# Kernel optimization log

Measured on AMD Instinct MI355X. Metric: run time of the kernel, lower is better.

The kernel has to match this reference:

```python
import jax, jax.numpy as jnp
import numpy as np

N = 50000
E = 800000
IN_DIM = 512
HID = 256
LAT = 128
K = 10
ALPHA = 0.1
BN_EPS = 1e-5


def setup_inputs() -> dict:
    key = jax.random.key(0)
    ks = jax.random.split(key, 6)
    x = jax.random.normal(ks[0], (N, IN_DIM), dtype=jnp.float32)
    edge_index = jax.random.randint(ks[1], (2, E), 0, N, dtype=jnp.int64)
    W_proj = jax.random.normal(ks[2], (IN_DIM, LAT), dtype=jnp.float32) * (IN_DIM ** -0.5)
    W1 = jax.random.normal(ks[3], (LAT, HID), dtype=jnp.float32) * (LAT ** -0.5)
    W2 = jax.random.normal(ks[4], (HID, LAT), dtype=jnp.float32) * (HID ** -0.5)
    return {
        "x": x, "edge_index": edge_index, "W_proj": W_proj,
        "W1": W1, "b1": jnp.zeros((HID,), jnp.float32),
        "gamma1": jnp.ones((HID,), jnp.float32), "beta1": jnp.zeros((HID,), jnp.float32),
        "mean1": jnp.zeros((HID,), jnp.float32), "var1": jnp.ones((HID,), jnp.float32),
        "W2": W2, "b2": jnp.zeros((LAT,), jnp.float32),
        "gamma2": jnp.ones((LAT,), jnp.float32), "beta2": jnp.zeros((LAT,), jnp.float32),
        "mean2": jnp.zeros((LAT,), jnp.float32), "var2": jnp.ones((LAT,), jnp.float32),
    }


def _gcn_norm(edge_index, n):
    # add self-loops, symmetric normalization D^-1/2 A D^-1/2 (PyG gcn_norm)
    loops = jnp.arange(n, dtype=edge_index.dtype)
    src = jnp.concatenate([edge_index[0], loops])
    dst = jnp.concatenate([edge_index[1], loops])
    deg = jax.ops.segment_sum(jnp.ones_like(dst, jnp.float32), dst, num_segments=n)
    dinv = jax.lax.rsqrt(jnp.maximum(deg, 1.0))  # deg >= 1 with self-loops
    norm = dinv[src] * dinv[dst]
    return src, dst, norm


def _propagate(h, src, dst, norm, n):
    # gather -> scale -> scatter-add: out[dst] += norm * h[src]
    return jax.ops.segment_sum(h[src] * norm[:, None], dst, num_segments=n)


def _bn(h, gamma, beta, mean, var):
    # BatchNorm1d in eval mode (running stats)
    return (h - mean) * jax.lax.rsqrt(var + BN_EPS) * gamma + beta


def reference(x, edge_index, W_proj, W1, b1, gamma1, beta1, mean1, var1,
              W2, b2, gamma2, beta2, mean2, var2):
    n = x.shape[0]
    src, dst, norm = _gcn_norm(edge_index, n)

    z0 = x @ W_proj                                   # [N, LAT]
    h1 = _propagate(z0 @ W1, src, dst, norm, n) + b1  # GCNConv 1
    h1 = jax.nn.relu(_bn(h1, gamma1, beta1, mean1, var1))
    h2 = _propagate(h1 @ W2, src, dst, norm, n) + b2  # GCNConv 2
    h2 = jax.nn.relu(_bn(h2, gamma2, beta2, mean2, var2))

    # APPNP: h_k = (1-alpha) * A_hat h_{k-1} + alpha * h_0
    def step(h, _):
        h = (1.0 - ALPHA) * _propagate(h, src, dst, norm, n) + ALPHA * h2
        return h, None
    z_refined, _ = jax.lax.scan(step, h2, None, length=K)

    z = z_refined + z0
    row, col = edge_index[0], edge_index[1]
    adj = jax.nn.sigmoid(jnp.sum(z[row] * z[col], axis=1))  # [E]
    return adj, z
```

## Files before the change

kernel.cpp:

```cpp
#include <hip/hip_runtime.h>

#define N_NODES 50000
#define N_EDGES 800000
#define IN_DIM  512
#define HID     256
#define LAT     128
#define K_ITERS 10
#define BN_EPS  1e-5f

typedef __attribute__((ext_vector_type(8))) short bf16x8;
typedef __attribute__((ext_vector_type(4))) float f32x4;

__device__ inline float bflo(unsigned v) { return __builtin_bit_cast(float, v << 16); }
__device__ inline float bfhi(unsigned v) { return __builtin_bit_cast(float, v & 0xffff0000u); }
__device__ inline unsigned f2bf_bits(float f)
{
    unsigned u = __builtin_bit_cast(unsigned, f);
    return (u + 0x7fffu + ((u >> 16) & 1u)) >> 16;
}
__device__ inline unsigned packbf(float x, float y)
{
    return f2bf_bits(x) | (f2bf_bits(y) << 16);
}

__global__ void detect_dtype_kernel(const int* __restrict__ ei32, int* __restrict__ flag)
{
    __shared__ int any;
    if (threadIdx.x == 0) any = 0;
    __syncthreads();
    int local = 0;
    for (int i = threadIdx.x; i < 4096; i += blockDim.x)
        local |= ei32[2 * i + 1];
    if (local) atomicOr(&any, 1);
    __syncthreads();
    if (threadIdx.x == 0) flag[0] = (any != 0) ? 1 : 0;
}

__global__ void init_cnt_kernel(int* __restrict__ cnt, int n)
{
    int i = blockIdx.x * blockDim.x + threadIdx.x;
    if (i < n) cnt[i] = 1;
}

__global__ void convert_count_kernel(const void* __restrict__ ei, const int* __restrict__ flag,
                                     int* __restrict__ srcE, int* __restrict__ dstE,
                                     int* __restrict__ cnt, int E)
{
    int e = blockIdx.x * blockDim.x + threadIdx.x;
    if (e >= E) return;
    int s, d;
    if (*flag) {
        const int* p = (const int*)ei;
        s = p[e]; d = p[E + e];
    } else {
        const long long* p = (const long long*)ei;
        s = (int)p[e]; d = (int)p[E + e];
    }
    srcE[e] = s;
    dstE[e] = d;
    atomicAdd(&cnt[d], 1);
}

__global__ __launch_bounds__(256) void block_sum_kernel(const int* __restrict__ cnt,
                                                        int* __restrict__ bsum, int n)
{
    __shared__ int s[256];
    int i = blockIdx.x * 256 + threadIdx.x;
    s[threadIdx.x] = (i < n) ? cnt[i] : 0;
    __syncthreads();
    for (int off = 128; off > 0; off >>= 1) {
        if (threadIdx.x < off) s[threadIdx.x] += s[threadIdx.x + off];
        __syncthreads();
    }
    if (threadIdx.x == 0) bsum[blockIdx.x] = s[0];
}

__global__ __launch_bounds__(256) void block_scan_kernel(int* __restrict__ bsum, int nb)
{
    __shared__ int s[256];
    int t = threadIdx.x;
    int v = (t < nb) ? bsum[t] : 0;
    s[t] = v;
    __syncthreads();
    for (int off = 1; off < 256; off <<= 1) {
        int u = (t >= off) ? s[t - off] : 0;
        __syncthreads();
        s[t] += u;
        __syncthreads();
    }
    if (t < nb) bsum[t] = s[t] - v;
}

__global__ __launch_bounds__(256) void final_scan_kernel(const int* __restrict__ cnt,
                                                         const int* __restrict__ bsum,
                                                         int* __restrict__ rowoff,
                                                         int* __restrict__ cursor,
                                                         float* __restrict__ dinv, int n)
{
    __shared__ int s[256];
    int t = threadIdx.x;
    int i = blockIdx.x * 256 + t;
    int c = (i < n) ? cnt[i] : 0;
    s[t] = c;
    __syncthreads();
    for (int off = 1; off < 256; off <<= 1) {
        int u = (t >= off) ? s[t - off] : 0;
        __syncthreads();
        s[t] += u;
        __syncthreads();
    }
    if (i < n) {
        int excl = bsum[blockIdx.x] + s[t] - c;
        rowoff[i] = excl;
        cursor[i] = excl;
        dinv[i] = rsqrtf((float)c);
    }
    if (i == 0) rowoff[n] = N_EDGES + N_NODES;
}

__global__ void scatter_kernel(const int* __restrict__ srcE, const int* __restrict__ dstE,
                               const float* __restrict__ dinv, int* __restrict__ cursor,
                               uint2* __restrict__ csr, int E, int n)
{
    int e = blockIdx.x * blockDim.x + threadIdx.x;
    if (e >= E + n) return;
    int s, d;
    if (e < E) { s = srcE[e]; d = dstE[e]; }
    else       { s = e - E;   d = s; }
    int pos = atomicAdd(&cursor[d], 1);
    float w = dinv[s] * dinv[d];
    csr[pos] = make_uint2((unsigned)s, __builtin_bit_cast(unsigned, w));
}

__global__ void transpose_cvt_kernel(const float* __restrict__ in, unsigned short* __restrict__ out,
                                     int R, int C)
{
    int idx = blockIdx.x * 256 + threadIdx.x;
    if (idx >= R * C) return;
    int c = idx / R, r = idx - c * R;
    out[idx] = (unsigned short)f2bf_bits(in[r * C + c]);
}

template<int KDIM, int COLS, int EPI, bool AF32>
__global__ __launch_bounds__(256) void gemm_mfma(const void* __restrict__ Ain,
                                                 const unsigned short* __restrict__ Bt,
                                                 unsigned short* __restrict__ Cout,
                                                 int M, int Nc,
                                                 const float* __restrict__ cb,
                                                 const float* __restrict__ cg,
                                                 const float* __restrict__ cbe,
                                                 const float* __restrict__ cm,
                                                 const float* __restrict__ cv)
{
    const int wave = threadIdx.x >> 6;
    const int lane = threadIdx.x & 63;
    const int s  = lane & 15;
    const int kc = lane >> 4;
    const int wrow0   = blockIdx.y * 64 + wave * 16;
    const int colbase = blockIdx.x * (16 * COLS);

    f32x4 acc[COLS] = {};

    const int arow = wrow0 + s;
    const bool aok = arow < M;

#pragma unroll 2
    for (int k0 = 0; k0 < KDIM; k0 += 32) {
        bf16x8 af = {};
        if (AF32) {
            if (aok) {
                const float* Ar = (const float*)Ain + (size_t)arow * KDIM + k0 + 8 * kc;
                float4 u0 = *(const float4*)Ar;
                float4 u1 = *(const float4*)(Ar + 4);
                af[0] = (short)f2bf_bits(u0.x); af[1] = (short)f2bf_bits(u0.y);
                af[2] = (short)f2bf_bits(u0.z); af[3] = (short)f2bf_bits(u0.w);
                af[4] = (short)f2bf_bits(u1.x); af[5] = (short)f2bf_bits(u1.y);
                af[6] = (short)f2bf_bits(u1.z); af[7] = (short)f2bf_bits(u1.w);
            }
        } else {
            if (aok)
                af = *(const bf16x8*)&((const unsigned short*)Ain)[(size_t)arow * KDIM + k0 + 8 * kc];
        }
#pragma unroll
        for (int t = 0; t < COLS; ++t) {
            const int bn = colbase + t * 16 + s;
            bf16x8 bf = *(const bf16x8*)&Bt[(size_t)bn * KDIM + k0 + 8 * kc];
            acc[t] = __builtin_amdgcn_mfma_f32_16x16x32_bf16(af, bf, acc[t], 0, 0, 0);
        }
    }

#pragma unroll
    for (int t = 0; t < COLS; ++t) {
        const int col = colbase + t * 16 + s;
        float sc = 1.f, sh = 0.f;
        if (EPI == 1) {
            sc = cg[col] * rsqrtf(cv[col] + BN_EPS);
            sh = (cb[col] - cm[col]) * sc + cbe[col];
        }
#pragma unroll
        for (int j = 0; j < 4; ++j) {
            const int crow = wrow0 + kc * 4 + j;
            if (crow < M) {
                float xv = acc[t][j];
                if (EPI == 1) xv = fmaxf(fmaf(xv, sc, sh), 0.f);
                Cout[(size_t)crow * Nc + col] = (unsigned short)f2bf_bits(xv);
            }
        }
    }
}

template<int MODE>
__global__ __launch_bounds__(256) void prop_row(const unsigned* __restrict__ in,
                                                const int* __restrict__ rowoff,
                                                const unsigned long long* __restrict__ csr,
                                                const unsigned* __restrict__ h2h,
                                                const unsigned* __restrict__ z0h,
                                                float* __restrict__ outf,
                                                unsigned* __restrict__ outh,
                                                const float* __restrict__ bb,
                                                const float* __restrict__ bg,
                                                const float* __restrict__ bbe,
                                                const float* __restrict__ bm,
                                                const float* __restrict__ bv)
{
    const int node = blockIdx.x * 4 + (threadIdx.x >> 6);
    const int lane = threadIdx.x & 63;
    const int g = lane >> 4, s = lane & 15;
    const int e0 = rowoff[node], e1 = rowoff[node + 1];

    float f[8] = {};
    int e = e0 + g;
    while (e < e1) {
        unsigned long long P[6];
        uint4 V[6];
#pragma unroll
        for (int i = 0; i < 6; ++i) { P[i] = 0; V[i] = make_uint4(0u, 0u, 0u, 0u); }
#pragma unroll
        for (int i = 0; i < 6; ++i)
            if (e + 4 * i < e1) P[i] = __builtin_nontemporal_load(&csr[e + 4 * i]);
#pragma unroll
        for (int i = 0; i < 6; ++i)
            if (e + 4 * i < e1) V[i] = *(const uint4*)&in[(size_t)(unsigned)P[i] * 64 + 4 * s];
#pragma unroll
        for (int i = 0; i < 6; ++i) {
            const float w = __builtin_bit_cast(float, (unsigned)(P[i] >> 32));
            f[0] = fmaf(w, bflo(V[i].x), f[0]); f[1] = fmaf(w, bfhi(V[i].x), f[1]);
            f[2] = fmaf(w, bflo(V[i].y), f[2]); f[3] = fmaf(w, bfhi(V[i].y), f[3]);
            f[4] = fmaf(w, bflo(V[i].z), f[4]); f[5] = fmaf(w, bfhi(V[i].z), f[5]);
            f[6] = fmaf(w, bflo(V[i].w), f[6]); f[7] = fmaf(w, bfhi(V[i].w), f[7]);
        }
        e += 24;
    }
#pragma unroll
    for (int i = 0; i < 8; ++i) {
        f[i] += __shfl_xor(f[i], 16, 64);
        f[i] += __shfl_xor(f[i], 32, 64);
    }

    if (g == 0) {
        const size_t o = (size_t)node * 64 + 4 * s;
        uint4 ov;
        if (MODE == 0) {
            ov.x = packbf(f[0], f[1]); ov.y = packbf(f[2], f[3]);
            ov.z = packbf(f[4], f[5]); ov.w = packbf(f[6], f[7]);
            *(uint4*)&outh[o] = ov;
        } else if (MODE == 1) {
            float4 G0 = *(const float4*)&bg[8 * s],  G1 = *(const float4*)&bg[8 * s + 4];
            float4 V0 = *(const float4*)&bv[8 * s],  V1 = *(const float4*)&bv[8 * s + 4];
            float4 B0 = *(const float4*)&bb[8 * s],  B1 = *(const float4*)&bb[8 * s + 4];
            float4 M0 = *(const float4*)&bm[8 * s],  M1 = *(const float4*)&bm[8 * s + 4];
            float4 E0 = *(const float4*)&bbe[8 * s], E1 = *(const float4*)&bbe[8 * s + 4];
            float gg[8] = {G0.x, G0.y, G0.z, G0.w, G1.x, G1.y, G1.z, G1.w};
            float vv[8] = {V0.x, V0.y, V0.z, V0.w, V1.x, V1.y, V1.z, V1.w};
            float bbv[8] = {B0.x, B0.y, B0.z, B0.w, B1.x, B1.y, B1.z, B1.w};
            float mm[8] = {M0.x, M0.y, M0.z, M0.w, M1.x, M1.y, M1.z, M1.w};
            float ee[8] = {E0.x, E0.y, E0.z, E0.w, E1.x, E1.y, E1.z, E1.w};
            float r[8];
#pragma unroll
            for (int i = 0; i < 8; ++i) {
                float sc = gg[i] * rsqrtf(vv[i] + BN_EPS);
                float sh = (bbv[i] - mm[i]) * sc + ee[i];
                r[i] = fmaxf(fmaf(f[i], sc, sh), 0.f);
            }
            ov.x = packbf(r[0], r[1]); ov.y = packbf(r[2], r[3]);
            ov.z = packbf(r[4], r[5]); ov.w = packbf(r[6], r[7]);
            *(uint4*)&outh[o] = ov;
        } else if (MODE == 2) {
            uint4 hv = *(const uint4*)&h2h[o];
            ov.x = packbf(fmaf(0.9f, f[0], 0.1f * bflo(hv.x)), fmaf(0.9f, f[1], 0.1f * bfhi(hv.x)));
            ov.y = packbf(fmaf(0.9f, f[2], 0.1f * bflo(hv.y)), fmaf(0.9f, f[3], 0.1f * bfhi(hv.y)));
            ov.z = packbf(fmaf(0.9f, f[4], 0.1f * bflo(hv.z)), fmaf(0.9f, f[5], 0.1f * bfhi(hv.z)));
            ov.w = packbf(fmaf(0.9f, f[6], 0.1f * bflo(hv.w)), fmaf(0.9f, f[7], 0.1f * bfhi(hv.w)));
            *(uint4*)&outh[o] = ov;
        } else {
            uint4 hv = *(const uint4*)&h2h[o];
            uint4 zv = *(const uint4*)&z0h[o];
            float r[8];
            r[0] = fmaf(0.9f, f[0], 0.1f * bflo(hv.x)) + bflo(zv.x);
            r[1] = fmaf(0.9f, f[1], 0.1f * bfhi(hv.x)) + bfhi(zv.x);
            r[2] = fmaf(0.9f, f[2], 0.1f * bflo(hv.y)) + bflo(zv.y);
            r[3] = fmaf(0.9f, f[3], 0.1f * bfhi(hv.y)) + bfhi(zv.y);
            r[4] = fmaf(0.9f, f[4], 0.1f * bflo(hv.z)) + bflo(zv.z);
            r[5] = fmaf(0.9f, f[5], 0.1f * bfhi(hv.z)) + bfhi(zv.z);
            r[6] = fmaf(0.9f, f[6], 0.1f * bflo(hv.w)) + bflo(zv.w);
            r[7] = fmaf(0.9f, f[7], 0.1f * bfhi(hv.w)) + bfhi(zv.w);
            *(float4*)&outf[(size_t)node * LAT + 8 * s]     = make_float4(r[0], r[1], r[2], r[3]);
            *(float4*)&outf[(size_t)node * LAT + 8 * s + 4] = make_float4(r[4], r[5], r[6], r[7]);
            ov.x = packbf(r[0], r[1]); ov.y = packbf(r[2], r[3]);
            ov.z = packbf(r[4], r[5]); ov.w = packbf(r[6], r[7]);
            *(uint4*)&outh[o] = ov;
        }
    }
}

__global__ __launch_bounds__(256) void edge_dot_mfma(const unsigned* __restrict__ zh,
                                                     const int* __restrict__ srcE,
                                                     const int* __restrict__ dstE,
                                                     float* __restrict__ adj)
{
    const int gw = blockIdx.x * 4 + (threadIdx.x >> 6);
    const int base = gw * 16;
    const int lane = threadIdx.x & 63;
    const int s = lane & 15, kc = lane >> 4;
    const int r = srcE[base + s];
    const int c = dstE[base + s];
    const unsigned* zr = &zh[(size_t)r * 64 + 4 * kc];
    const unsigned* zc = &zh[(size_t)c * 64 + 4 * kc];
    f32x4 acc = {};
#pragma unroll
    for (int k0 = 0; k0 < 4; ++k0) {
        bf16x8 af = *(const bf16x8*)(zr + 16 * k0);
        bf16x8 bf = *(const bf16x8*)(zc + 16 * k0);
        acc = __builtin_amdgcn_mfma_f32_16x16x32_bf16(af, bf, acc, 0, 0, 0);
    }
    if ((s >> 2) == kc) {
        const int j = s & 3;
        float v = (j == 0) ? acc[0] : (j == 1) ? acc[1] : (j == 2) ? acc[2] : acc[3];
        adj[base + s] = 1.f / (1.f + expf(-v));
    }
}

extern "C" void kernel_launch(void* const* d_in, const int* in_sizes, int n_in,
                              void* d_out, int out_size, void* d_ws, size_t ws_size,
                              hipStream_t stream)
{
    const float* x     = (const float*)d_in[0];
    const void*  ei    = d_in[1];
    const float* Wproj = (const float*)d_in[2];
    const float* W1    = (const float*)d_in[3];
    const float* b1    = (const float*)d_in[4];
    const float* g1    = (const float*)d_in[5];
    const float* be1   = (const float*)d_in[6];
    const float* m1    = (const float*)d_in[7];
    const float* v1    = (const float*)d_in[8];
    const float* W2    = (const float*)d_in[9];
    const float* b2    = (const float*)d_in[10];
    const float* g2    = (const float*)d_in[11];
    const float* be2   = (const float*)d_in[12];
    const float* m2    = (const float*)d_in[13];
    const float* v2    = (const float*)d_in[14];

    float* out_adj = (float*)d_out;
    float* out_z   = (float*)d_out + N_EDGES;

    char* w = (char*)d_ws;
    size_t off = 0;
    auto alloc = [&](size_t bytes) {
        void* p = w + off;
        off += (bytes + 255) & ~(size_t)255;
        return p;
    };
    const size_t NB = (size_t)N_NODES * 64 * 4;
    const int NBLK = (N_NODES + 255) / 256;

    int*            flag   = (int*)           alloc(4);
    int*            cnt    = (int*)           alloc((size_t)N_NODES * 4);
    int*            cursor = (int*)           alloc((size_t)N_NODES * 4);
    int*            rowoff = (int*)           alloc((size_t)(N_NODES + 1) * 4);
    float*          dinv   = (float*)         alloc((size_t)N_NODES * 4);
    int*            bsum   = (int*)           alloc(256 * 4);
    int*            srcE   = (int*)           alloc((size_t)N_EDGES * 4);
    int*            dstE   = (int*)           alloc((size_t)N_EDGES * 4);
    uint2*          csr    = (uint2*)         alloc((size_t)(N_EDGES + N_NODES) * 8);
    unsigned short* Wpt    = (unsigned short*)alloc((size_t)LAT * IN_DIM * 2);
    unsigned short* W1t    = (unsigned short*)alloc((size_t)HID * LAT * 2);
    unsigned short* W2t    = (unsigned short*)alloc((size_t)LAT * HID * 2);
    unsigned*       z0h    = (unsigned*)      alloc(NB);
    unsigned*       p0h    = (unsigned*)      alloc(NB);
    unsigned short* h1h    = (unsigned short*)alloc(2 * NB);
    unsigned*       t2h    = (unsigned*)      alloc(NB);
    unsigned*       h2h    = (unsigned*)      alloc(NB);

    unsigned* pingA = (unsigned*)h1h;
    unsigned* pingB = (unsigned*)h1h + N_NODES * 64;

    detect_dtype_kernel<<<1, 256, 0, stream>>>((const int*)ei, flag);
    init_cnt_kernel<<<(N_NODES + 255) / 256, 256, 0, stream>>>(cnt, N_NODES);
    convert_count_kernel<<<(N_EDGES + 255) / 256, 256, 0, stream>>>(ei, flag, srcE, dstE, cnt, N_EDGES);
    block_sum_kernel<<<NBLK, 256, 0, stream>>>(cnt, bsum, N_NODES);
    block_scan_kernel<<<1, 256, 0, stream>>>(bsum, NBLK);
    final_scan_kernel<<<NBLK, 256, 0, stream>>>(cnt, bsum, rowoff, cursor, dinv, N_NODES);
    scatter_kernel<<<(N_EDGES + N_NODES + 255) / 256, 256, 0, stream>>>(srcE, dstE, dinv, cursor,
                                                                        csr, N_EDGES, N_NODES);

    transpose_cvt_kernel<<<(IN_DIM * LAT + 255) / 256, 256, 0, stream>>>(Wproj, Wpt, IN_DIM, LAT);
    transpose_cvt_kernel<<<(LAT * HID + 255) / 256, 256, 0, stream>>>(W1, W1t, LAT, HID);
    transpose_cvt_kernel<<<(HID * LAT + 255) / 256, 256, 0, stream>>>(W2, W2t, HID, LAT);

    const int gy = (N_NODES + 63) / 64;
    const int pgrid = N_NODES / 4;

    gemm_mfma<IN_DIM, 4, 0, true><<<dim3(2, gy), 256, 0, stream>>>(x, Wpt, (unsigned short*)z0h,
                                                                   N_NODES, LAT,
                                                                   nullptr, nullptr, nullptr, nullptr, nullptr);
    prop_row<0><<<pgrid, 256, 0, stream>>>(z0h, rowoff, (const unsigned long long*)csr,
                                           nullptr, nullptr, nullptr, p0h,
                                           nullptr, nullptr, nullptr, nullptr, nullptr);
    gemm_mfma<LAT, 4, 1, false><<<dim3(4, gy), 256, 0, stream>>>(p0h, W1t, h1h, N_NODES, HID,
                                                                 b1, g1, be1, m1, v1);
    gemm_mfma<HID, 4, 0, false><<<dim3(2, gy), 256, 0, stream>>>(h1h, W2t, (unsigned short*)t2h,
                                                                 N_NODES, LAT,
                                                                 nullptr, nullptr, nullptr, nullptr, nullptr);
    prop_row<1><<<pgrid, 256, 0, stream>>>(t2h, rowoff, (const unsigned long long*)csr,
                                           nullptr, nullptr, nullptr, h2h,
                                           b2, g2, be2, m2, v2);

    const unsigned* cur = h2h;
    for (int it = 0; it < K_ITERS; ++it) {
        if (it == K_ITERS - 1) {
            prop_row<3><<<pgrid, 256, 0, stream>>>(cur, rowoff, (const unsigned long long*)csr,
                                                   h2h, z0h, out_z, z0h,
                                                   nullptr, nullptr, nullptr, nullptr, nullptr);
        } else {
            unsigned* nxt = (it & 1) ? pingB : pingA;
            prop_row<2><<<pgrid, 256, 0, stream>>>(cur, rowoff, (const unsigned long long*)csr,
                                                   h2h, nullptr, nullptr, nxt,
                                                   nullptr, nullptr, nullptr, nullptr, nullptr);
            cur = nxt;
        }
    }

    edge_dot_mfma<<<N_EDGES / 64, 256, 0, stream>>>(z0h, srcE, dstE, out_adj);
}
```

Before: 769.0 us.

## Software-pipeline GEMM loads with register prefetch and widen column tile

Replaces the GEMM kernel with a version in which each wave computes 8 column tiles (128 columns) rather than 4. It prefetches several A k-slices into registers and double-buffers the B fragments so global loads overlap the MFMA work. Out-of-range A rows are clamped instead of branched on, and the grids shrink to match. Separately, the CSR load in the propagation kernel switches from a nontemporal load to a normal cached load. The changes trade higher register pressure, and possibly lower occupancy, for better latency hiding and half as many redundant A reads.

```diff
diff --git a/kernel.cpp b/kernel.cpp
--- a/kernel.cpp
+++ b/kernel.cpp
@@ -141,8 +141,8 @@
     out[idx] = (unsigned short)f2bf_bits(in[r * C + c]);
 }
 
-template<int KDIM, int COLS, int EPI, bool AF32>
-__global__ __launch_bounds__(256) void gemm_mfma(const void* __restrict__ Ain,
+template<int KDIM, int EPI, bool AF32>
+__global__ __launch_bounds__(256) void gemm_pipe(const void* __restrict__ Ain,
                                                  const unsigned short* __restrict__ Bt,
                                                  unsigned short* __restrict__ Cout,
                                                  int M, int Nc,
@@ -152,45 +152,69 @@
                                                  const float* __restrict__ cm,
                                                  const float* __restrict__ cv)
 {
+    constexpr int NK = KDIM / 32;
+    constexpr int PREF = AF32 ? (NK < 4 ? NK : 4) : (NK < 8 ? NK : 8);
     const int wave = threadIdx.x >> 6;
     const int lane = threadIdx.x & 63;
     const int s  = lane & 15;
     const int kc = lane >> 4;
     const int wrow0   = blockIdx.y * 64 + wave * 16;
-    const int colbase = blockIdx.x * (16 * COLS);
-
-    f32x4 acc[COLS] = {};
-
-    const int arow = wrow0 + s;
-    const bool aok = arow < M;
-
-#pragma unroll 2
-    for (int k0 = 0; k0 < KDIM; k0 += 32) {
-        bf16x8 af = {};
-        if (AF32) {
-            if (aok) {
-                const float* Ar = (const float*)Ain + (size_t)arow * KDIM + k0 + 8 * kc;
-                float4 u0 = *(const float4*)Ar;
-                float4 u1 = *(const float4*)(Ar + 4);
-                af[0] = (short)f2bf_bits(u0.x); af[1] = (short)f2bf_bits(u0.y);
-                af[2] = (short)f2bf_bits(u0.z); af[3] = (short)f2bf_bits(u0.w);
-                af[4] = (short)f2bf_bits(u1.x); af[5] = (short)f2bf_bits(u1.y);
-                af[6] = (short)f2bf_bits(u1.z); af[7] = (short)f2bf_bits(u1.w);
+    const int colbase = blockIdx.x * 128;
+    int arow = wrow0 + s; if (arow > M - 1) arow = M - 1;
+
+    const float*          Af = (const float*)Ain + (size_t)arow * KDIM + 8 * kc;
+    const unsigned short* Ah = (const unsigned short*)Ain + (size_t)arow * KDIM + 8 * kc;
+    const unsigned short* Bp = Bt + (size_t)(colbase + s) * KDIM + 8 * kc;
+
+    float4 Araw[AF32 ? PREF : 1][2];
+    bf16x8 Areg[AF32 ? 1 : PREF];
+    bf16x8 Breg[2][8];
+    f32x4  acc[8] = {};
+
+#pragma unroll
+    for (int i = 0; i < PREF; ++i) {
+        if constexpr (AF32) {
+            Araw[i][0] = *(const float4*)(Af + 32 * i);
+            Araw[i][1] = *(const float4*)(Af + 32 * i + 4);
+        } else {
+            Areg[i] = *(const bf16x8*)(Ah + 32 * i);
+        }
+    }
+#pragma unroll
+    for (int t = 0; t < 8; ++t)
+        Breg[0][t] = *(const bf16x8*)(Bp + (size_t)16 * t * KDIM);
+
+#pragma unroll
+    for (int k = 0; k < NK; ++k) {
+        if (k + 1 < NK) {
+#pragma unroll
+            for (int t = 0; t < 8; ++t)
+                Breg[(k + 1) & 1][t] = *(const bf16x8*)(Bp + (size_t)16 * t * KDIM + 32 * (k + 1));
+        }
+        bf16x8 af;
+        if constexpr (AF32) {
+            float4 u0 = Araw[k % PREF][0];
+            float4 u1 = Araw[k % PREF][1];
+            if (k + PREF < NK) {
+                Araw[k % PREF][0] = *(const float4*)(Af + 32 * (k + PREF));
+                Araw[k % PREF][1] = *(const float4*)(Af + 32 * (k + PREF) + 4);
             }
+            af[0] = (short)f2bf_bits(u0.x); af[1] = (short)f2bf_bits(u0.y);
+            af[2] = (short)f2bf_bits(u0.z); af[3] = (short)f2bf_bits(u0.w);
+            af[4] = (short)f2bf_bits(u1.x); af[5] = (short)f2bf_bits(u1.y);
+            af[6] = (short)f2bf_bits(u1.z); af[7] = (short)f2bf_bits(u1.w);
         } else {
-            if (aok)
-                af = *(const bf16x8*)&((const unsigned short*)Ain)[(size_t)arow * KDIM + k0 + 8 * kc];
-        }
-#pragma unroll
-        for (int t = 0; t < COLS; ++t) {
-            const int bn = colbase + t * 16 + s;
-            bf16x8 bf = *(const bf16x8*)&Bt[(size_t)bn * KDIM + k0 + 8 * kc];
-            acc[t] = __builtin_amdgcn_mfma_f32_16x16x32_bf16(af, bf, acc[t], 0, 0, 0);
-        }
-    }
-
-#pragma unroll
-    for (int t = 0; t < COLS; ++t) {
+            af = Areg[k % PREF];
+            if (k + PREF < NK)
+                Areg[k % PREF] = *(const bf16x8*)(Ah + 32 * (k + PREF));
+        }
+#pragma unroll
+        for (int t = 0; t < 8; ++t)
+            acc[t] = __builtin_amdgcn_mfma_f32_16x16x32_bf16(af, Breg[k & 1][t], acc[t], 0, 0, 0);
+    }
+
+#pragma unroll
+    for (int t = 0; t < 8; ++t) {
         const int col = colbase + t * 16 + s;
         float sc = 1.f, sh = 0.f;
         if (EPI == 1) {
@@ -237,7 +261,7 @@
         for (int i = 0; i < 6; ++i) { P[i] = 0; V[i] = make_uint4(0u, 0u, 0u, 0u); }
 #pragma unroll
         for (int i = 0; i < 6; ++i)
-            if (e + 4 * i < e1) P[i] = __builtin_nontemporal_load(&csr[e + 4 * i]);
+            if (e + 4 * i < e1) P[i] = csr[e + 4 * i];
 #pragma unroll
         for (int i = 0; i < 6; ++i)
             if (e + 4 * i < e1) V[i] = *(const uint4*)&in[(size_t)(unsigned)P[i] * 64 + 4 * s];
@@ -410,17 +434,17 @@
     const int gy = (N_NODES + 63) / 64;
     const int pgrid = N_NODES / 4;
 
-    gemm_mfma<IN_DIM, 4, 0, true><<<dim3(2, gy), 256, 0, stream>>>(x, Wpt, (unsigned short*)z0h,
-                                                                   N_NODES, LAT,
-                                                                   nullptr, nullptr, nullptr, nullptr, nullptr);
+    gemm_pipe<IN_DIM, 0, true><<<dim3(1, gy), 256, 0, stream>>>(x, Wpt, (unsigned short*)z0h,
+                                                                N_NODES, LAT,
+                                                                nullptr, nullptr, nullptr, nullptr, nullptr);
     prop_row<0><<<pgrid, 256, 0, stream>>>(z0h, rowoff, (const unsigned long long*)csr,
                                            nullptr, nullptr, nullptr, p0h,
                                            nullptr, nullptr, nullptr, nullptr, nullptr);
-    gemm_mfma<LAT, 4, 1, false><<<dim3(4, gy), 256, 0, stream>>>(p0h, W1t, h1h, N_NODES, HID,
-                                                                 b1, g1, be1, m1, v1);
-    gemm_mfma<HID, 4, 0, false><<<dim3(2, gy), 256, 0, stream>>>(h1h, W2t, (unsigned short*)t2h,
-                                                                 N_NODES, LAT,
-                                                                 nullptr, nullptr, nullptr, nullptr, nullptr);
+    gemm_pipe<LAT, 1, false><<<dim3(2, gy), 256, 0, stream>>>(p0h, W1t, h1h, N_NODES, HID,
+                                                              b1, g1, be1, m1, v1);
+    gemm_pipe<HID, 0, false><<<dim3(1, gy), 256, 0, stream>>>(h1h, W2t, (unsigned short*)t2h,
+                                                              N_NODES, LAT,
+                                                              nullptr, nullptr, nullptr, nullptr, nullptr);
     prop_row<1><<<pgrid, 256, 0, stream>>>(t2h, rowoff, (const unsigned long long*)csr,
                                            nullptr, nullptr, nullptr, h2h,
                                            b2, g2, be2, m2, v2);
```

Result: faster. 719.7 us, median of 2 (-6.4%).
